# Optimization experiments

Hardware: AMD Instinct MI355X
Metric: run time of the kernel (lower is better)

## Reference

```python
import jax, jax.numpy as jnp
import numpy as np

N, K, P_DIM, HID, NCLS = 20000, 16, 63, 32 + 0, 32
HID = 128
IN_DIM = P_DIM + 1


def setup_inputs() -> dict:
    key = jax.random.key(0)
    ks = iter(jax.random.split(key, 64))

    def nrm(shape, s=0.1):
        return jax.random.normal(next(ks), shape, jnp.float32) * s

    inp = {
        "p": nrm((N, P_DIM), 1.0),
        "neigh_idx": jax.random.randint(next(ks), (N, K), 0, N, dtype=jnp.int32),
    }
    dims = [(IN_DIM, HID), (HID, HID), (HID, NCLS)]
    for l, (din, dout) in enumerate(dims):
        inp[f"l{l}_Wih"] = nrm((4 * din, din))
        inp[f"l{l}_Whh"] = nrm((4 * din, din))
        inp[f"l{l}_bih"] = jnp.zeros((4 * din,), jnp.float32)
        inp[f"l{l}_bhh"] = jnp.zeros((4 * din,), jnp.float32)
        inp[f"l{l}_Wself"] = nrm((dout, din))
        inp[f"l{l}_Wneigh"] = nrm((dout, din))
        inp[f"l{l}_b"] = jnp.zeros((dout,), jnp.float32)
    return inp


def _lstm_agg(feat, neigh_idx, Wih, Whh, bih, bhh):
    # Per-node LSTM over the K in-neighbor features (DGL _lstm_reducer).
    n, h_dim = feat.shape[0], Whh.shape[1]
    bias = bih + bhh

    def step(carry, idx_t):
        h, c = carry
        x = feat[idx_t]                                   # [N, Din] gather (step t message)
        g = x @ Wih.T + h @ Whh.T + bias                  # [N, 4H]
        i, f, gg, o = jnp.split(g, 4, axis=-1)            # torch LSTM gate order i,f,g,o
        c = jax.nn.sigmoid(f) * c + jax.nn.sigmoid(i) * jnp.tanh(gg)
        h = jax.nn.sigmoid(o) * jnp.tanh(c)
        return (h, c), None

    init = (jnp.zeros((n, h_dim), feat.dtype), jnp.zeros((n, h_dim), feat.dtype))
    (h, _), _ = jax.lax.scan(step, init, neigh_idx.T)     # scan over K neighbor slots
    return h                                              # final hidden state = neigh feat


def _forward(p, neigh_idx, *params):
    # features = cat(in_degree/N, p); fixed-degree graph -> in_degree == K
    deg = jnp.full((p.shape[0], 1), K / N, p.dtype)
    feat = jnp.concatenate([deg, p], axis=1)
    layers = [params[7 * l: 7 * (l + 1)] for l in range(3)]
    for l, (Wih, Whh, bih, bhh, Wself, Wneigh, b) in enumerate(layers):
        neigh = _lstm_agg(feat, neigh_idx, Wih, Whh, bih, bhh)
        feat = feat @ Wself.T + neigh @ Wneigh.T + b      # fc_self + fc_neigh + bias
        if l < 2:
            feat = jax.nn.relu(feat)
    return feat


def reference(p, neigh_idx,
              l0_Wih, l0_Whh, l0_bih, l0_bhh, l0_Wself, l0_Wneigh, l0_b,
              l1_Wih, l1_Whh, l1_bih, l1_bhh, l1_Wself, l1_Wneigh, l1_b,
              l2_Wih, l2_Whh, l2_bih, l2_bhh, l2_Wself, l2_Wneigh, l2_b):
    return _forward(p, neigh_idx,
                    l0_Wih, l0_Whh, l0_bih, l0_bhh, l0_Wself, l0_Wneigh, l0_b,
                    l1_Wih, l1_Whh, l1_bih, l1_bhh, l1_Wself, l1_Wneigh, l1_b,
                    l2_Wih, l2_Whh, l2_bih, l2_bhh, l2_Wself, l2_Wneigh, l2_b)
```

## Files before the change

### kernel.cpp

```cpp
#include <hip/hip_runtime.h>
#include <hip/hip_bf16.h>
#include <stdint.h>


#define N_NODES 20000
#define KNE 16

typedef __bf16 bf16x8 __attribute__((ext_vector_type(8)));
typedef float f32x4 __attribute__((ext_vector_type(4)));

__device__ __forceinline__ bf16x8 ldb8(const __hip_bfloat16* p) {
  uint4 u = *reinterpret_cast<const uint4*>(p);
  return __builtin_bit_cast(bf16x8, u);
}
__device__ __forceinline__ void pin(bf16x8& v) {
  uint4 u = __builtin_bit_cast(uint4, v);
  asm volatile("" : "+v"(u.x), "+v"(u.y), "+v"(u.z), "+v"(u.w));
  v = __builtin_bit_cast(bf16x8, u);
}
__device__ __forceinline__ float b2f_lo(uint32_t u) {
  return __builtin_bit_cast(float, u << 16);
}
__device__ __forceinline__ float b2f_hi(uint32_t u) {
  return __builtin_bit_cast(float, u & 0xffff0000u);
}
__device__ __forceinline__ uint32_t pk2(float a, float b) {
  uint32_t ua = (uint32_t)__builtin_bit_cast(unsigned short, __float2bfloat16(a));
  uint32_t ub = (uint32_t)__builtin_bit_cast(unsigned short, __float2bfloat16(b));
  return ua | (ub << 16);
}
__device__ __forceinline__ float sigf(float x) {
  float t = __builtin_amdgcn_exp2f(-1.442695041f * x);
  return __builtin_amdgcn_rcpf(1.f + t);
}
__device__ __forceinline__ float tanhf_(float x) {
  float t = __builtin_amdgcn_exp2f(2.885390082f * x);
  return 1.f - 2.f * __builtin_amdgcn_rcpf(t + 1.f);
}

__global__ void build_feat0(const float* __restrict__ p,
                            __hip_bfloat16* __restrict__ f0) {
  int i = blockIdx.x * 256 + threadIdx.x;
  if (i >= N_NODES * 64) return;
  int n = i >> 6, c = i & 63;
  float v = (c == 0) ? ((float)KNE / (float)N_NODES) : p[n * 63 + c - 1];
  f0[i] = __float2bfloat16(v);
}

__global__ void cvt4(const float* __restrict__ s0, int n0,
                     const float* __restrict__ s1, int n1,
                     const float* __restrict__ s2, int n2,
                     const float* __restrict__ s3, int n3,
                     __hip_bfloat16* __restrict__ d0,
                     __hip_bfloat16* __restrict__ d1,
                     __hip_bfloat16* __restrict__ d2,
                     __hip_bfloat16* __restrict__ d3) {
  int i = blockIdx.x * 256 + threadIdx.x;
  if (i < n0) { d0[i] = __float2bfloat16(s0[i]); return; }
  i -= n0;
  if (i < n1) { d1[i] = __float2bfloat16(s1[i]); return; }
  i -= n1;
  if (i < n2) { d2[i] = __float2bfloat16(s2[i]); return; }
  i -= n2;
  if (i < n3) d3[i] = __float2bfloat16(s3[i]);
}

template <int DIN, int DOUT>
__global__ __launch_bounds__(256, 2) void proj_kern(
    const __hip_bfloat16* __restrict__ feat,
    const __hip_bfloat16* __restrict__ Wih,
    const float* __restrict__ bih,
    const float* __restrict__ bhh,
    const __hip_bfloat16* __restrict__ Wself,
    const float* __restrict__ bvec,
    __hip_bfloat16* __restrict__ P, float* __restrict__ S) {
  constexpr int KB = DIN / 32;
  constexpr int CCT = DIN / 16;
  constexpr int CTS = DOUT / 16;
  const int n0 = blockIdx.x * 32;
  const int tid = threadIdx.x;
  const int wv = tid >> 6;
  const int lane = tid & 63;
  const int quad = lane >> 4;
  const int c16 = lane & 15;

  bf16x8 afr[2][KB];
#pragma unroll
  for (int rt = 0; rt < 2; ++rt)
#pragma unroll
    for (int kb = 0; kb < KB; ++kb)
      afr[rt][kb] =
          ldb8(feat + (size_t)(n0 + rt * 16 + c16) * DIN + kb * 32 + quad * 8);

  const f32x4 zz = {0.f, 0.f, 0.f, 0.f};
  for (int ct = wv; ct < CCT + CTS; ct += 4) {
    if (ct < CCT) {
      const int cc = ct * 16 + c16;
      f32x4 ag[4][2];
#pragma unroll
      for (int g = 0; g < 4; ++g) { ag[g][0] = zz; ag[g][1] = zz; }
#pragma unroll
      for (int kb = 0; kb < KB; ++kb)
#pragma unroll
        for (int g = 0; g < 4; ++g) {
          bf16x8 b = ldb8(Wih + (size_t)(g * DIN + cc) * DIN + kb * 32 +
                          quad * 8);
          ag[g][0] = __builtin_amdgcn_mfma_f32_16x16x32_bf16(afr[0][kb], b,
                                                             ag[g][0], 0, 0, 0);
          ag[g][1] = __builtin_amdgcn_mfma_f32_16x16x32_bf16(afr[1][kb], b,
                                                             ag[g][1], 0, 0, 0);
        }
      float bi = bih[cc] + bhh[cc];
      float bff = bih[DIN + cc] + bhh[DIN + cc];
      float bg = bih[2 * DIN + cc] + bhh[2 * DIN + cc];
      float bo = bih[3 * DIN + cc] + bhh[3 * DIN + cc];
      uint2* Pp = reinterpret_cast<uint2*>(P);
#pragma unroll
      for (int rt = 0; rt < 2; ++rt)
#pragma unroll
        for (int r = 0; r < 4; ++r) {
          int n = n0 + rt * 16 + quad * 4 + r;
          uint2 u;
          u.x = pk2(ag[0][rt][r] + bi, ag[1][rt][r] + bff);
          u.y = pk2(ag[2][rt][r] + bg, ag[3][rt][r] + bo);
          Pp[(size_t)n * DIN + cc] = u;
        }
    } else {
      const int c = (ct - CCT) * 16 + c16;
      f32x4 a0 = zz, a1 = zz;
#pragma unroll
      for (int kb = 0; kb < KB; ++kb) {
        bf16x8 b = ldb8(Wself + (size_t)c * DIN + kb * 32 + quad * 8);
        a0 = __builtin_amdgcn_mfma_f32_16x16x32_bf16(afr[0][kb], b, a0, 0, 0, 0);
        a1 = __builtin_amdgcn_mfma_f32_16x16x32_bf16(afr[1][kb], b, a1, 0, 0, 0);
      }
      float bias = bvec[c];
#pragma unroll
      for (int r = 0; r < 4; ++r) {
        S[(size_t)(n0 + quad * 4 + r) * DOUT + c] = a0[r] + bias;
        S[(size_t)(n0 + 16 + quad * 4 + r) * DOUT + c] = a1[r] + bias;
      }
    }
  }
}

template <int DIN, int DOUT, bool RELU, typename OutT>
__global__ __launch_bounds__((DIN / 16) * 64)
__attribute__((amdgpu_waves_per_eu(4))) void lstm_fc_kern(
    const __hip_bfloat16* __restrict__ P,
    const float* __restrict__ S,
    const __hip_bfloat16* __restrict__ Whh,
    const __hip_bfloat16* __restrict__ Wng,
    const int* __restrict__ nidx,
    OutT* __restrict__ outp) {
  constexpr int W = DIN / 16;
  constexpr int KB = DIN / 32;
  constexpr int HS = DIN + 8;

  __shared__ __align__(16) __hip_bfloat16 hl[2][16 * HS];
  __shared__ int idxl[16 * KNE];

  const int n0 = blockIdx.x * 16;
  const int tid = threadIdx.x;
  const int wv = tid >> 6;
  const int lane = tid & 63;
  const int quad = lane >> 4;
  const int c16 = lane & 15;
  const int col = wv * 16 + c16;

  for (int i = tid; i < 16 * KNE; i += W * 64) idxl[i] = nidx[n0 * KNE + i];
  __syncthreads();

  uint2 pf[2][4];
  auto loadpf = [&](int t, int b) {
#pragma unroll
    for (int r = 0; r < 4; ++r) {
      int src = idxl[(quad * 4 + r) * KNE + t];
      pf[b][r] =
          reinterpret_cast<const uint2*>(P + (size_t)src * (4 * DIN))[col];
    }
  };

  loadpf(0, 0);

  bf16x8 Bp[4][KB];
#pragma unroll
  for (int g = 0; g < 4; ++g)
#pragma unroll
    for (int kb = 0; kb < KB; ++kb) {
      Bp[g][kb] =
          ldb8(Whh + (size_t)(g * DIN + col) * DIN + kb * 32 + quad * 8);
      pin(Bp[g][kb]);
    }

  loadpf(1, 1);

  float cst[4];
#pragma unroll
  for (int r = 0; r < 4; ++r) cst[r] = 0.f;

  auto initag = [&](int b, f32x4 (&ag)[4]) {
#pragma unroll
    for (int r = 0; r < 4; ++r) {
      ag[0][r] = b2f_lo(pf[b][r].x);
      ag[1][r] = b2f_hi(pf[b][r].x);
      ag[2][r] = b2f_lo(pf[b][r].y);
      ag[3][r] = b2f_hi(pf[b][r].y);
    }
  };

  auto gates = [&](int hb, const f32x4 (&ag)[4]) {
#pragma unroll
    for (int r = 0; r < 4; ++r) {
      float cc = sigf(ag[1][r]) * cst[r] + sigf(ag[0][r]) * tanhf_(ag[2][r]);
      cst[r] = cc;
      hl[hb][(quad * 4 + r) * HS + col] =
          __float2bfloat16(sigf(ag[3][r]) * tanhf_(cc));
    }
  };

  {
    f32x4 ag[4];
    initag(0, ag);
    gates(0, ag);
  }

#pragma unroll
  for (int t = 1; t < KNE; ++t) {
    __syncthreads();
    if (t + 1 < KNE) loadpf(t + 1, (t + 1) & 1);
    const int pb = (t - 1) & 1;
    bf16x8 Af[KB];
#pragma unroll
    for (int kb = 0; kb < KB; ++kb)
      Af[kb] = ldb8(&hl[pb][c16 * HS + kb * 32 + quad * 8]);
    f32x4 ag[4];
    initag(t & 1, ag);
#pragma unroll
    for (int kb = 0; kb < KB; ++kb)
#pragma unroll
      for (int g = 0; g < 4; ++g)
        ag[g] = __builtin_amdgcn_mfma_f32_16x16x32_bf16(Af[kb], Bp[g][kb],
                                                        ag[g], 0, 0, 0);
    gates(t & 1, ag);
  }

  const f32x4 zz = {0.f, 0.f, 0.f, 0.f};
  __syncthreads();
  bf16x8 Hf[KB];
#pragma unroll
  for (int kb = 0; kb < KB; ++kb)
    Hf[kb] = ldb8(&hl[1][c16 * HS + kb * 32 + quad * 8]);
  for (int ct = wv; ct < DOUT / 16; ct += W) {
    f32x4 a = zz;
#pragma unroll
    for (int kb = 0; kb < KB; ++kb) {
      bf16x8 b = ldb8(Wng + (size_t)(ct * 16 + c16) * DIN + kb * 32 + quad * 8);
      a = __builtin_amdgcn_mfma_f32_16x16x32_bf16(Hf[kb], b, a, 0, 0, 0);
    }
#pragma unroll
    for (int r = 0; r < 4; ++r) {
      int n = n0 + quad * 4 + r;
      int c = ct * 16 + c16;
      float v = a[r] + S[(size_t)n * DOUT + c];
      if (RELU) v = fmaxf(v, 0.f);
      if constexpr (sizeof(OutT) == 2)
        outp[(size_t)n * DOUT + c] = __float2bfloat16(v);
      else
        outp[(size_t)n * DOUT + c] = v;
    }
  }
}

extern "C" void kernel_launch(void* const* d_in, const int* in_sizes, int n_in,
                              void* d_out, int out_size, void* d_ws,
                              size_t ws_size, hipStream_t stream) {
  (void)in_sizes; (void)n_in; (void)out_size; (void)ws_size;
  const float* p = (const float*)d_in[0];
  const int* nidx = (const int*)d_in[1];
  const float* L[3][7];
  for (int l = 0; l < 3; ++l)
    for (int j = 0; j < 7; ++j)
      L[l][j] = (const float*)d_in[2 + 7 * l + j];

  char* w = (char*)d_ws;
  __hip_bfloat16* feat0 = (__hip_bfloat16*)(w);
  __hip_bfloat16* feat1 = (__hip_bfloat16*)(w + 2560000);
  __hip_bfloat16* feat2 = (__hip_bfloat16*)(w + 7680000);
  __hip_bfloat16* Pb    = (__hip_bfloat16*)(w + 12800000);
  float*          Sb    = (float*)(w + 33280000);
  __hip_bfloat16* wb    = (__hip_bfloat16*)(w + 43520000);

  const int din_[3] = {64, 128, 128}, dout_[3] = {128, 128, 32};
  __hip_bfloat16 *Wih_b[3], *Whh_b[3], *Wself_b[3], *Wng_b[3];
  size_t off = 0;
  for (int l = 0; l < 3; ++l) {
    int din = din_[l], dout = dout_[l];
    Wih_b[l] = wb + off;   off += (size_t)4 * din * din;
    Whh_b[l] = wb + off;   off += (size_t)4 * din * din;
    Wself_b[l] = wb + off; off += (size_t)dout * din;
    Wng_b[l] = wb + off;   off += (size_t)dout * din;
  }
  for (int l = 0; l < 3; ++l) {
    int din = din_[l], dout = dout_[l];
    int n0 = 4 * din * din, n2 = dout * din;
    int tot = 2 * n0 + 2 * n2;
    cvt4<<<(tot + 255) / 256, 256, 0, stream>>>(
        L[l][0], n0, L[l][1], n0, L[l][4], n2, L[l][5], n2,
        Wih_b[l], Whh_b[l], Wself_b[l], Wng_b[l]);
  }

  build_feat0<<<(N_NODES * 64 + 255) / 256, 256, 0, stream>>>(p, feat0);

  proj_kern<64, 128><<<N_NODES / 32, 256, 0, stream>>>(
      feat0, Wih_b[0], L[0][2], L[0][3], Wself_b[0], L[0][6], Pb, Sb);
  lstm_fc_kern<64, 128, true, __hip_bfloat16>
      <<<N_NODES / 16, 256, 0, stream>>>(Pb, Sb, Whh_b[0], Wng_b[0], nidx,
                                         feat1);

  proj_kern<128, 128><<<N_NODES / 32, 256, 0, stream>>>(
      feat1, Wih_b[1], L[1][2], L[1][3], Wself_b[1], L[1][6], Pb, Sb);
  lstm_fc_kern<128, 128, true, __hip_bfloat16>
      <<<N_NODES / 16, 512, 0, stream>>>(Pb, Sb, Whh_b[1], Wng_b[1], nidx,
                                         feat2);

  proj_kern<128, 32><<<N_NODES / 32, 256, 0, stream>>>(
      feat2, Wih_b[2], L[2][2], L[2][3], Wself_b[2], L[2][6], Pb, Sb);
  lstm_fc_kern<128, 32, false, float>
      <<<N_NODES / 16, 512, 0, stream>>>(Pb, Sb, Whh_b[2], Wng_b[2], nidx,
                                         (float*)d_out);
}
```

Baseline: 344.6 us.

## Process two node tiles per block in layer-0 LSTM and merge weight conversions

Adds an NT template parameter so each LSTM block handles NT groups of 16 nodes, reusing the register-pinned Whh fragments across tiles. Layer 0 uses NT=2 with half as many blocks, which gives more independent MFMA chains per barrier step. The three per-layer weight-conversion launches are merged into one cvt_all kernel to cut launch overhead. The trade-off is more registers and LDS per block, and fewer blocks for layer 0.

```diff
diff --git a/kernel.cpp b/kernel.cpp
--- a/kernel.cpp
+++ b/kernel.cpp
@@ -47,22 +47,20 @@
   f0[i] = __float2bfloat16(v);
 }
 
-__global__ void cvt4(const float* __restrict__ s0, int n0,
-                     const float* __restrict__ s1, int n1,
-                     const float* __restrict__ s2, int n2,
-                     const float* __restrict__ s3, int n3,
-                     __hip_bfloat16* __restrict__ d0,
-                     __hip_bfloat16* __restrict__ d1,
-                     __hip_bfloat16* __restrict__ d2,
-                     __hip_bfloat16* __restrict__ d3) {
+struct CvtArgs {
+  const float* s[12];
+  __hip_bfloat16* d[12];
+  int off[13];
+};
+__global__ void cvt_all(CvtArgs a) {
   int i = blockIdx.x * 256 + threadIdx.x;
-  if (i < n0) { d0[i] = __float2bfloat16(s0[i]); return; }
-  i -= n0;
-  if (i < n1) { d1[i] = __float2bfloat16(s1[i]); return; }
-  i -= n1;
-  if (i < n2) { d2[i] = __float2bfloat16(s2[i]); return; }
-  i -= n2;
-  if (i < n3) d3[i] = __float2bfloat16(s3[i]);
+  if (i >= a.off[12]) return;
+#pragma unroll
+  for (int k = 0; k < 12; ++k)
+    if (i >= a.off[k] && i < a.off[k + 1]) {
+      int j = i - a.off[k];
+      a.d[k][j] = __float2bfloat16(a.s[k][j]);
+    }
 }
 
 template <int DIN, int DOUT>
@@ -144,7 +142,7 @@
   }
 }
 
-template <int DIN, int DOUT, bool RELU, typename OutT>
+template <int DIN, int DOUT, int NT, bool RELU, typename OutT>
 __global__ __launch_bounds__((DIN / 16) * 64)
 __attribute__((amdgpu_waves_per_eu(4))) void lstm_fc_kern(
     const __hip_bfloat16* __restrict__ P,
@@ -156,11 +154,12 @@
   constexpr int W = DIN / 16;
   constexpr int KB = DIN / 32;
   constexpr int HS = DIN + 8;
-
-  __shared__ __align__(16) __hip_bfloat16 hl[2][16 * HS];
-  __shared__ int idxl[16 * KNE];
-
-  const int n0 = blockIdx.x * 16;
+  constexpr int NN = 16 * NT;
+
+  __shared__ __align__(16) __hip_bfloat16 hl[2][NN * HS];
+  __shared__ int idxl[NN * KNE];
+
+  const int n0 = blockIdx.x * NN;
   const int tid = threadIdx.x;
   const int wv = tid >> 6;
   const int lane = tid & 63;
@@ -168,17 +167,19 @@
   const int c16 = lane & 15;
   const int col = wv * 16 + c16;
 
-  for (int i = tid; i < 16 * KNE; i += W * 64) idxl[i] = nidx[n0 * KNE + i];
+  for (int i = tid; i < NN * KNE; i += W * 64) idxl[i] = nidx[n0 * KNE + i];
   __syncthreads();
 
-  uint2 pf[2][4];
+  uint2 pf[2][NT][4];
   auto loadpf = [&](int t, int b) {
 #pragma unroll
-    for (int r = 0; r < 4; ++r) {
-      int src = idxl[(quad * 4 + r) * KNE + t];
-      pf[b][r] =
-          reinterpret_cast<const uint2*>(P + (size_t)src * (4 * DIN))[col];
-    }
+    for (int nt = 0; nt < NT; ++nt)
+#pragma unroll
+      for (int r = 0; r < 4; ++r) {
+        int src = idxl[(nt * 16 + quad * 4 + r) * KNE + t];
+        pf[b][nt][r] =
+            reinterpret_cast<const uint2*>(P + (size_t)src * (4 * DIN))[col];
+      }
   };
 
   loadpf(0, 0);
@@ -195,34 +196,38 @@
 
   loadpf(1, 1);
 
-  float cst[4];
-#pragma unroll
-  for (int r = 0; r < 4; ++r) cst[r] = 0.f;
-
-  auto initag = [&](int b, f32x4 (&ag)[4]) {
+  float cst[NT][4];
+#pragma unroll
+  for (int nt = 0; nt < NT; ++nt)
+#pragma unroll
+    for (int r = 0; r < 4; ++r) cst[nt][r] = 0.f;
+
+  auto initag = [&](int b, int nt, f32x4 (&ag)[4]) {
 #pragma unroll
     for (int r = 0; r < 4; ++r) {
-      ag[0][r] = b2f_lo(pf[b][r].x);
-      ag[1][r] = b2f_hi(pf[b][r].x);
-      ag[2][r] = b2f_lo(pf[b][r].y);
-      ag[3][r] = b2f_hi(pf[b][r].y);
+      ag[0][r] = b2f_lo(pf[b][nt][r].x);
+      ag[1][r] = b2f_hi(pf[b][nt][r].x);
+      ag[2][r] = b2f_lo(pf[b][nt][r].y);
+      ag[3][r] = b2f_hi(pf[b][nt][r].y);
     }
   };
 
-  auto gates = [&](int hb, const f32x4 (&ag)[4]) {
+  auto gates = [&](int hb, int nt, const f32x4 (&ag)[4]) {
 #pragma unroll
     for (int r = 0; r < 4; ++r) {
-      float cc = sigf(ag[1][r]) * cst[r] + sigf(ag[0][r]) * tanhf_(ag[2][r]);
-      cst[r] = cc;
-      hl[hb][(quad * 4 + r) * HS + col] =
+      float cc =
+          sigf(ag[1][r]) * cst[nt][r] + sigf(ag[0][r]) * tanhf_(ag[2][r]);
+      cst[nt][r] = cc;
+      hl[hb][(nt * 16 + quad * 4 + r) * HS + col] =
           __float2bfloat16(sigf(ag[3][r]) * tanhf_(cc));
     }
   };
 
-  {
+#pragma unroll
+  for (int nt = 0; nt < NT; ++nt) {
     f32x4 ag[4];
-    initag(0, ag);
-    gates(0, ag);
+    initag(0, nt, ag);
+    gates(0, nt, ag);
   }
 
 #pragma unroll
@@ -230,45 +235,57 @@
     __syncthreads();
     if (t + 1 < KNE) loadpf(t + 1, (t + 1) & 1);
     const int pb = (t - 1) & 1;
-    bf16x8 Af[KB];
-#pragma unroll
-    for (int kb = 0; kb < KB; ++kb)
-      Af[kb] = ldb8(&hl[pb][c16 * HS + kb * 32 + quad * 8]);
-    f32x4 ag[4];
-    initag(t & 1, ag);
-#pragma unroll
-    for (int kb = 0; kb < KB; ++kb)
-#pragma unroll
-      for (int g = 0; g < 4; ++g)
-        ag[g] = __builtin_amdgcn_mfma_f32_16x16x32_bf16(Af[kb], Bp[g][kb],
-                                                        ag[g], 0, 0, 0);
-    gates(t & 1, ag);
+#pragma unroll
+    for (int nt = 0; nt < NT; ++nt) {
+      bf16x8 Af[KB];
+#pragma unroll
+      for (int kb = 0; kb < KB; ++kb)
+        Af[kb] = ldb8(&hl[pb][(nt * 16 + c16) * HS + kb * 32 + quad * 8]);
+      f32x4 ag[4];
+      initag(t & 1, nt, ag);
+#pragma unroll
+      for (int kb = 0; kb < KB; ++kb)
+#pragma unroll
+        for (int g = 0; g < 4; ++g)
+          ag[g] = __builtin_amdgcn_mfma_f32_16x16x32_bf16(Af[kb], Bp[g][kb],
+                                                          ag[g], 0, 0, 0);
+      gates(t & 1, nt, ag);
+    }
   }
 
   const f32x4 zz = {0.f, 0.f, 0.f, 0.f};
   __syncthreads();
-  bf16x8 Hf[KB];
-#pragma unroll
-  for (int kb = 0; kb < KB; ++kb)
-    Hf[kb] = ldb8(&hl[1][c16 * HS + kb * 32 + quad * 8]);
+  bf16x8 Hf[NT][KB];
+#pragma unroll
+  for (int nt = 0; nt < NT; ++nt)
+#pragma unroll
+    for (int kb = 0; kb < KB; ++kb)
+      Hf[nt][kb] = ldb8(&hl[1][(nt * 16 + c16) * HS + kb * 32 + quad * 8]);
   for (int ct = wv; ct < DOUT / 16; ct += W) {
-    f32x4 a = zz;
+    f32x4 a[NT];
+#pragma unroll
+    for (int nt = 0; nt < NT; ++nt) a[nt] = zz;
 #pragma unroll
     for (int kb = 0; kb < KB; ++kb) {
       bf16x8 b = ldb8(Wng + (size_t)(ct * 16 + c16) * DIN + kb * 32 + quad * 8);
-      a = __builtin_amdgcn_mfma_f32_16x16x32_bf16(Hf[kb], b, a, 0, 0, 0);
-    }
-#pragma unroll
-    for (int r = 0; r < 4; ++r) {
-      int n = n0 + quad * 4 + r;
-      int c = ct * 16 + c16;
-      float v = a[r] + S[(size_t)n * DOUT + c];
-      if (RELU) v = fmaxf(v, 0.f);
-      if constexpr (sizeof(OutT) == 2)
-        outp[(size_t)n * DOUT + c] = __float2bfloat16(v);
-      else
-        outp[(size_t)n * DOUT + c] = v;
-    }
+#pragma unroll
+      for (int nt = 0; nt < NT; ++nt)
+        a[nt] = __builtin_amdgcn_mfma_f32_16x16x32_bf16(Hf[nt][kb], b, a[nt],
+                                                        0, 0, 0);
+    }
+#pragma unroll
+    for (int nt = 0; nt < NT; ++nt)
+#pragma unroll
+      for (int r = 0; r < 4; ++r) {
+        int n = n0 + nt * 16 + quad * 4 + r;
+        int c = ct * 16 + c16;
+        float v = a[nt][r] + S[(size_t)n * DOUT + c];
+        if (RELU) v = fmaxf(v, 0.f);
+        if constexpr (sizeof(OutT) == 2)
+          outp[(size_t)n * DOUT + c] = __float2bfloat16(v);
+        else
+          outp[(size_t)n * DOUT + c] = v;
+      }
   }
 }
 
@@ -293,40 +310,47 @@
 
   const int din_[3] = {64, 128, 128}, dout_[3] = {128, 128, 32};
   __hip_bfloat16 *Wih_b[3], *Whh_b[3], *Wself_b[3], *Wng_b[3];
+  CvtArgs ca;
   size_t off = 0;
-  for (int l = 0; l < 3; ++l) {
-    int din = din_[l], dout = dout_[l];
-    Wih_b[l] = wb + off;   off += (size_t)4 * din * din;
-    Whh_b[l] = wb + off;   off += (size_t)4 * din * din;
-    Wself_b[l] = wb + off; off += (size_t)dout * din;
-    Wng_b[l] = wb + off;   off += (size_t)dout * din;
-  }
+  int k = 0, pre = 0;
   for (int l = 0; l < 3; ++l) {
     int din = din_[l], dout = dout_[l];
     int n0 = 4 * din * din, n2 = dout * din;
-    int tot = 2 * n0 + 2 * n2;
-    cvt4<<<(tot + 255) / 256, 256, 0, stream>>>(
-        L[l][0], n0, L[l][1], n0, L[l][4], n2, L[l][5], n2,
-        Wih_b[l], Whh_b[l], Wself_b[l], Wng_b[l]);
-  }
-
+    Wih_b[l] = wb + off;   off += (size_t)n0;
+    Whh_b[l] = wb + off;   off += (size_t)n0;
+    Wself_b[l] = wb + off; off += (size_t)n2;
+    Wng_b[l] = wb + off;   off += (size_t)n2;
+    const float* srcs[4] = {L[l][0], L[l][1], L[l][4], L[l][5]};
+    __hip_bfloat16* dsts[4] = {Wih_b[l], Whh_b[l], Wself_b[l], Wng_b[l]};
+    int ns[4] = {n0, n0, n2, n2};
+    for (int j = 0; j < 4; ++j) {
+      ca.s[k] = srcs[j];
+      ca.d[k] = dsts[j];
+      ca.off[k] = pre;
+      pre += ns[j];
+      ++k;
+    }
+  }
+  ca.off[12] = pre;
+
+  cvt_all<<<(pre + 255) / 256, 256, 0, stream>>>(ca);
   build_feat0<<<(N_NODES * 64 + 255) / 256, 256, 0, stream>>>(p, feat0);
 
   proj_kern<64, 128><<<N_NODES / 32, 256, 0, stream>>>(
       feat0, Wih_b[0], L[0][2], L[0][3], Wself_b[0], L[0][6], Pb, Sb);
-  lstm_fc_kern<64, 128, true, __hip_bfloat16>
-      <<<N_NODES / 16, 256, 0, stream>>>(Pb, Sb, Whh_b[0], Wng_b[0], nidx,
+  lstm_fc_kern<64, 128, 2, true, __hip_bfloat16>
+      <<<N_NODES / 32, 256, 0, stream>>>(Pb, Sb, Whh_b[0], Wng_b[0], nidx,
                                          feat1);
 
   proj_kern<128, 128><<<N_NODES / 32, 256, 0, stream>>>(
       feat1, Wih_b[1], L[1][2], L[1][3], Wself_b[1], L[1][6], Pb, Sb);
-  lstm_fc_kern<128, 128, true, __hip_bfloat16>
+  lstm_fc_kern<128, 128, 1, true, __hip_bfloat16>
       <<<N_NODES / 16, 512, 0, stream>>>(Pb, Sb, Whh_b[1], Wng_b[1], nidx,
                                          feat2);
 
   proj_kern<128, 32><<<N_NODES / 32, 256, 0, stream>>>(
       feat2, Wih_b[2], L[2][2], L[2][3], Wself_b[2], L[2][6], Pb, Sb);
-  lstm_fc_kern<128, 32, false, float>
+  lstm_fc_kern<128, 32, 1, false, float>
       <<<N_NODES / 16, 512, 0, stream>>>(Pb, Sb, Whh_b[2], Wng_b[2], nidx,
                                          (float*)d_out);
 }
```

Result: no change. 347.2 us (+0.7%).
